# Kernel tuning notes

Hardware: AMD Instinct MI355X
Metric: run time of the kernel (lower is better)

The kernel has to match this reference:

```python
import jax, jax.numpy as jnp
import numpy as np

NUM_HIDDEN = 2048
NUM_CLASSES = 10
SEQ_LEN = 128
BATCH = 512


def setup_inputs() -> dict:
    key = jax.random.key(0)
    ks = jax.random.split(key, 6)
    # kaiming-uniform-ish init scales (exact init is irrelevant for correctness testing)
    def ku(k, shape, fan_in):
        bound = float(np.sqrt(6.0 / fan_in))
        return jax.random.uniform(k, shape, jnp.float32, -bound, bound)
    return {
        "x": jax.random.normal(ks[0], (BATCH, SEQ_LEN), jnp.float32),
        "weighthx": ku(ks[1], (NUM_HIDDEN, 1), 1),
        "weighthh": ku(ks[2], (NUM_HIDDEN, NUM_HIDDEN), NUM_HIDDEN),
        "bh": ku(ks[3], (NUM_HIDDEN, 1), 1),
        "weightph": ku(ks[4], (NUM_CLASSES, NUM_HIDDEN), NUM_HIDDEN),
        "bp": ku(ks[5], (NUM_CLASSES, 1), 1),
    }


def reference(x, weighthx, weighthh, bh, weightph, bp):
    # x: [B, S]; hidden state h: [H, B] as in the torch code
    B = x.shape[0]
    h0 = jnp.zeros((weighthh.shape[0], B), dtype=x.dtype)

    def step(h, xt):
        # xt: [B]; weighthx: [H, 1] -> input contribution [H, B]
        h_new = jnp.tanh(weighthx @ xt[None, :] + weighthh @ h + bh)
        return h_new, None

    h_final, _ = jax.lax.scan(step, h0, x.T)  # scan over S
    out = weightph @ h_final + bp  # [C, B]
    return out.T  # [B, C]
```

## Files before the change

### kernel.cpp

```cpp
#include <hip/hip_runtime.h>
#include <hip/hip_cooperative_groups.h>

#define HID 2048
#define BAT 512
#define SEQ 128
#define NCLS 10

typedef __attribute__((ext_vector_type(4))) float f32x4;
typedef __attribute__((ext_vector_type(8))) short s16x8;
typedef __attribute__((ext_vector_type(4))) unsigned short u16x4;

__device__ __forceinline__ float bf2f(unsigned short u) {
  union { unsigned int i; float f; } v;
  v.i = ((unsigned int)u) << 16;
  return v.f;
}
__device__ __forceinline__ unsigned short f2bf(float f) {
  union { float f; unsigned int i; } v;
  v.f = f;
  unsigned int u = v.i;
  return (unsigned short)((u + 0x7fffu + ((u >> 16) & 1u)) >> 16);
}

__global__ __launch_bounds__(256) void cvt_kernel(const float* __restrict__ src,
                                                  unsigned short* __restrict__ dst,
                                                  int n) {
  int i = (blockIdx.x * 256 + threadIdx.x) * 4;
  if (i + 3 < n) {
    f32x4 v = *(const f32x4*)(src + i);
    u16x4 o;
    o.x = f2bf(v.x);
    o.y = f2bf(v.y);
    o.z = f2bf(v.z);
    o.w = f2bf(v.w);
    *(u16x4*)(dst + i) = o;
  }
}

__global__ __launch_bounds__(256) void xpose_kernel(const float* __restrict__ x,
                                                    float* __restrict__ xT) {
  const int t = blockIdx.x;
  for (int b = threadIdx.x; b < BAT; b += 256)
    xT[t * BAT + b] = x[b * SEQ + t];
}

__device__ __forceinline__ void gload16(const void* g, void* l) {
  __builtin_amdgcn_global_load_lds(
      (const __attribute__((address_space(1))) unsigned int*)g,
      (__attribute__((address_space(3))) unsigned int*)l, 16, 0, 0);
}
__device__ __forceinline__ void gload16_dev(const void* g, void* l) {
  __builtin_amdgcn_global_load_lds(
      (const __attribute__((address_space(1))) unsigned int*)g,
      (__attribute__((address_space(3))) unsigned int*)l, 16, 0, 0x10);
}

__global__ __launch_bounds__(256) void rnn_kernel(
    const unsigned short* __restrict__ W,
    unsigned short* __restrict__ h0,
    unsigned short* __restrict__ h1,
    const float* __restrict__ whx,
    const float* __restrict__ bh,
    const float* __restrict__ xT,
    unsigned int* __restrict__ cnt) {
  __shared__ unsigned short ldsA[4][64 * 64];
  __shared__ unsigned short ldsB[4][64 * 64];

  const int tid = threadIdx.x;
  const int wave = tid >> 6;
  const int lane = tid & 63;
  const int id = blockIdx.x;
  const int g = id >> 5;
  const int m0 = (id & 31) * 64;
  const int n0 = g * 64;
  const int wm = wave >> 1;
  const int wn = wave & 1;
  const int fl = lane & 15;
  const int hi = lane >> 4;

  const int r0 = tid >> 3;
  const int r1 = 32 + r0;
  const int c0 = (tid & 7) ^ (r0 & 7);
  const int c1 = (tid & 7) ^ (r1 & 7);
  const unsigned short* gA0 = W + (size_t)(m0 + r0) * HID + c0 * 8;
  const unsigned short* gA1 = W + (size_t)(m0 + r1) * HID + c1 * 8;
  const size_t bo0 = (size_t)(n0 + r0) * HID + c0 * 8;
  const size_t bo1 = (size_t)(n0 + r1) * HID + c1 * 8;
  const int ldst = wave * 512;

  int offA[2][2], offB[2][2];
#pragma unroll
  for (int f = 0; f < 2; ++f) {
#pragma unroll
    for (int ks = 0; ks < 2; ++ks) {
      const int ra = wm * 32 + f * 16 + fl;
      const int rb = wn * 32 + f * 16 + fl;
      const int ch = ks * 4 + hi;
      offA[f][ks] = ra * 64 + ((ch ^ (ra & 7)) * 8);
      offB[f][ks] = rb * 64 + ((ch ^ (rb & 7)) * 8);
    }
  }

  const int mbase = m0 + wm * 32;
  const int nbase = n0 + wn * 32;
  f32x4 wxv[2], bvv[2];
#pragma unroll
  for (int mf = 0; mf < 2; ++mf) {
    wxv[mf] = *(const f32x4*)&whx[mbase + mf * 16 + hi * 4];
    bvv[mf] = *(const f32x4*)&bh[mbase + mf * 16 + hi * 4];
  }

  unsigned short* const A0 = ldsA[0]; unsigned short* const B0 = ldsB[0];
  unsigned short* const A1 = ldsA[1]; unsigned short* const B1 = ldsB[1];
  unsigned short* const A2 = ldsA[2]; unsigned short* const B2 = ldsB[2];
  unsigned short* const A3 = ldsA[3]; unsigned short* const B3 = ldsB[3];

#define STAGE(kk, ab, bb)                        \
  do {                                           \
    gload16(gA0 + (kk), (ab) + ldst);            \
    gload16(gA1 + (kk), (ab) + 2048 + ldst);     \
    gload16_dev(gB0 + (kk), (bb) + ldst);        \
    gload16_dev(gB1 + (kk), (bb) + 2048 + ldst); \
  } while (0)

#define COMPUTE(ab, bb)                                                                  \
  do {                                                                                   \
    _Pragma("unroll") for (int ks = 0; ks < 2; ++ks) {                                   \
      s16x8 a0 = *(const s16x8*)&(ab)[offA[0][ks]];                                      \
      s16x8 a1 = *(const s16x8*)&(ab)[offA[1][ks]];                                      \
      s16x8 b0 = *(const s16x8*)&(bb)[offB[0][ks]];                                      \
      s16x8 b1 = *(const s16x8*)&(bb)[offB[1][ks]];                                      \
      acc[0][0] = __builtin_amdgcn_mfma_f32_16x16x32_bf16(a0, b0, acc[0][0], 0, 0, 0);   \
      acc[0][1] = __builtin_amdgcn_mfma_f32_16x16x32_bf16(a0, b1, acc[0][1], 0, 0, 0);   \
      acc[1][0] = __builtin_amdgcn_mfma_f32_16x16x32_bf16(a1, b0, acc[1][0], 0, 0, 0);   \
      acc[1][1] = __builtin_amdgcn_mfma_f32_16x16x32_bf16(a1, b1, acc[1][1], 0, 0, 0);   \
    }                                                                                    \
  } while (0)

#define WAITB(n) \
  asm volatile("s_waitcnt vmcnt(" #n ") lgkmcnt(0)\n\ts_barrier" ::: "memory")

  for (int t = 0; t < SEQ; ++t) {
    const unsigned short* hin = (t & 1) ? h1 : h0;
    unsigned short* hout = (t & 1) ? h0 : h1;
    const unsigned short* gB0 = hin + bo0;
    const unsigned short* gB1 = hin + bo1;

    f32x4 acc[2][2] = {};

    STAGE(0, A0, B0);
    STAGE(64, A1, B1);
    STAGE(128, A2, B2);
    WAITB(8);

#pragma unroll 1
    for (int kb = 0; kb < 28; kb += 4) {
      const int k4 = kb * 64;
      STAGE(k4 + 192, A3, B3); COMPUTE(A0, B0); WAITB(8);
      STAGE(k4 + 256, A0, B0); COMPUTE(A1, B1); WAITB(8);
      STAGE(k4 + 320, A1, B1); COMPUTE(A2, B2); WAITB(8);
      STAGE(k4 + 384, A2, B2); COMPUTE(A3, B3); WAITB(8);
    }
    STAGE(1984, A3, B3);
    COMPUTE(A0, B0); WAITB(8);
    COMPUTE(A1, B1); WAITB(4);
    COMPUTE(A2, B2); WAITB(0);
    COMPUTE(A3, B3);

#pragma unroll
    for (int mf = 0; mf < 2; ++mf) {
      const int mrow = mbase + mf * 16 + hi * 4;
#pragma unroll
      for (int nf = 0; nf < 2; ++nf) {
        const int ncol = nbase + nf * 16 + fl;
        const float xv = xT[t * BAT + ncol];
        u16x4 o;
#pragma unroll
        for (int j = 0; j < 4; ++j) {
          float z = acc[mf][nf][j] + wxv[mf][j] * xv + bvv[mf][j];
          o[j] = f2bf(tanhf(z));
        }
        union { u16x4 v; unsigned long long u; } pun;
        pun.v = o;
        const unsigned long long addr =
            (unsigned long long)&hout[(size_t)ncol * HID + mrow];
        asm volatile("global_store_dwordx2 %0, %1, off sc1"
                     :: "v"(addr), "v"(pun.u) : "memory");
      }
    }

    if (t != SEQ - 1) {
      asm volatile("s_waitcnt vmcnt(0)" ::: "memory");
      __syncthreads();
      if (tid == 0) {
        __hip_atomic_fetch_add(&cnt[g * 16], 1u, __ATOMIC_RELAXED,
                               __HIP_MEMORY_SCOPE_AGENT);
        const unsigned int target = 32u * (unsigned)(t + 1);
        while (__hip_atomic_load(&cnt[g * 16], __ATOMIC_RELAXED,
                                 __HIP_MEMORY_SCOPE_AGENT) < target)
          __builtin_amdgcn_s_sleep(1);
      }
      __syncthreads();
    }
  }
#undef STAGE
#undef COMPUTE
#undef WAITB
}

__global__ __launch_bounds__(256) void proj_kernel(const unsigned short* __restrict__ hT,
                                                   const float* __restrict__ wp,
                                                   const float* __restrict__ bp,
                                                   float* __restrict__ out) {
  const int b = blockIdx.x;
  const int wave = threadIdx.x >> 6;
  const int lane = threadIdx.x & 63;
  for (int c = wave; c < NCLS; c += 4) {
    float s = 0.f;
    for (int k = lane * 8; k < HID; k += 512) {
      s16x8 hv = *(const s16x8*)&hT[b * HID + k];
      f32x4 w0 = *(const f32x4*)&wp[c * HID + k];
      f32x4 w1 = *(const f32x4*)&wp[c * HID + k + 4];
      s += w0.x * bf2f((unsigned short)hv[0]) + w0.y * bf2f((unsigned short)hv[1]) +
           w0.z * bf2f((unsigned short)hv[2]) + w0.w * bf2f((unsigned short)hv[3]) +
           w1.x * bf2f((unsigned short)hv[4]) + w1.y * bf2f((unsigned short)hv[5]) +
           w1.z * bf2f((unsigned short)hv[6]) + w1.w * bf2f((unsigned short)hv[7]);
    }
#pragma unroll
    for (int off = 32; off > 0; off >>= 1) s += __shfl_down(s, off);
    if (lane == 0) out[b * NCLS + c] = s + bp[c];
  }
}

extern "C" void kernel_launch(void* const* d_in, const int* in_sizes, int n_in,
                              void* d_out, int out_size, void* d_ws, size_t ws_size,
                              hipStream_t stream) {
  (void)in_sizes; (void)n_in; (void)out_size; (void)ws_size;
  const float* x   = (const float*)d_in[0];
  const float* whx = (const float*)d_in[1];
  const float* whh = (const float*)d_in[2];
  const float* bh  = (const float*)d_in[3];
  const float* wp  = (const float*)d_in[4];
  const float* bp  = (const float*)d_in[5];
  float* out = (float*)d_out;

  unsigned short* Wb = (unsigned short*)d_ws;
  unsigned short* h0 = Wb + (size_t)HID * HID;
  unsigned short* h1 = h0 + (size_t)BAT * HID;
  float* xT = (float*)(h1 + (size_t)BAT * HID);
  unsigned int* cnt = (unsigned int*)(xT + (size_t)SEQ * BAT);

  cvt_kernel<<<dim3((HID * HID) / 1024), 256, 0, stream>>>(whh, Wb, HID * HID);
  xpose_kernel<<<dim3(SEQ), 256, 0, stream>>>(x, xT);
  hipMemsetAsync(h0, 0, (size_t)BAT * HID * sizeof(unsigned short), stream);
  hipMemsetAsync(cnt, 0, 8 * 64, stream);

  const unsigned short* Wb_c = Wb;
  unsigned short* h0_p = h0;
  unsigned short* h1_p = h1;
  const float* whx_p = whx;
  const float* bh_p = bh;
  const float* xT_p = xT;
  unsigned int* cnt_p = cnt;
  void* args[] = {(void*)&Wb_c, (void*)&h0_p, (void*)&h1_p,
                  (void*)&whx_p, (void*)&bh_p, (void*)&xT_p, (void*)&cnt_p};
  hipLaunchCooperativeKernel((const void*)rnn_kernel, dim3(256), dim3(256),
                             args, 0, stream);

  proj_kernel<<<dim3(BAT), 256, 0, stream>>>(h0, wp, bp, out);
}
```

Baseline: 2.282 ms.

## Keep weight slab resident in LDS and stream hidden state from global into registers

Each block now loads its 32-row slice of the recurrent weight matrix into LDS once, before the time loop. The per-step work reads the hidden state from global memory directly into registers with software prefetch, so the weights are no longer re-streamed from global every step. The grid is repartitioned to 64 row-slices by 4 batch groups of 128 columns, and barrier targets change from 32 to 64 blocks per group. The sc1 inline-asm stores and per-step vmcnt waits are replaced with plain stores plus threadfences. The risks are that the hidden-state loads may not hit cache efficiently, the 128KB LDS allocation may limit occupancy or exceed limits, and the new fence semantics add ordering cost.

```diff
diff --git a/kernel.cpp b/kernel.cpp
--- a/kernel.cpp
+++ b/kernel.cpp
@@ -49,11 +49,6 @@
       (const __attribute__((address_space(1))) unsigned int*)g,
       (__attribute__((address_space(3))) unsigned int*)l, 16, 0, 0);
 }
-__device__ __forceinline__ void gload16_dev(const void* g, void* l) {
-  __builtin_amdgcn_global_load_lds(
-      (const __attribute__((address_space(1))) unsigned int*)g,
-      (__attribute__((address_space(3))) unsigned int*)l, 16, 0, 0x10);
-}
 
 __global__ __launch_bounds__(256) void rnn_kernel(
     const unsigned short* __restrict__ W,
@@ -63,116 +58,107 @@
     const float* __restrict__ bh,
     const float* __restrict__ xT,
     unsigned int* __restrict__ cnt) {
-  __shared__ unsigned short ldsA[4][64 * 64];
-  __shared__ unsigned short ldsB[4][64 * 64];
+  __shared__ unsigned short ldsW[32 * HID];
 
   const int tid = threadIdx.x;
   const int wave = tid >> 6;
   const int lane = tid & 63;
   const int id = blockIdx.x;
-  const int g = id >> 5;
-  const int m0 = (id & 31) * 64;
-  const int n0 = g * 64;
-  const int wm = wave >> 1;
-  const int wn = wave & 1;
+  const int mp = id >> 2;
+  const int g = id & 3;
+  const int n0 = g * 128;
   const int fl = lane & 15;
   const int hi = lane >> 4;
 
-  const int r0 = tid >> 3;
-  const int r1 = 32 + r0;
-  const int c0 = (tid & 7) ^ (r0 & 7);
-  const int c1 = (tid & 7) ^ (r1 & 7);
-  const unsigned short* gA0 = W + (size_t)(m0 + r0) * HID + c0 * 8;
-  const unsigned short* gA1 = W + (size_t)(m0 + r1) * HID + c1 * 8;
-  const size_t bo0 = (size_t)(n0 + r0) * HID + c0 * 8;
-  const size_t bo1 = (size_t)(n0 + r1) * HID + c1 * 8;
-  const int ldst = wave * 512;
-
-  int offA[2][2], offB[2][2];
-#pragma unroll
-  for (int f = 0; f < 2; ++f) {
+  {
+    const unsigned short* wp0 = W + (size_t)mp * 32 * HID;
+    for (int i = 0; i < 32; ++i) {
+      gload16(wp0 + (size_t)i * HID + ((tid ^ (i & 7)) * 8),
+              ldsW + i * HID + wave * 512);
+    }
+    asm volatile("s_waitcnt vmcnt(0)" ::: "memory");
+    __syncthreads();
+  }
+
+  int oA[2][2];
+#pragma unroll
+  for (int mf = 0; mf < 2; ++mf)
 #pragma unroll
     for (int ks = 0; ks < 2; ++ks) {
-      const int ra = wm * 32 + f * 16 + fl;
-      const int rb = wn * 32 + f * 16 + fl;
-      const int ch = ks * 4 + hi;
-      offA[f][ks] = ra * 64 + ((ch ^ (ra & 7)) * 8);
-      offB[f][ks] = rb * 64 + ((ch ^ (rb & 7)) * 8);
-    }
-  }
-
-  const int mbase = m0 + wm * 32;
-  const int nbase = n0 + wn * 32;
+      const int row = mf * 16 + fl;
+      oA[mf][ks] = row * HID + (((ks * 4 + hi) ^ (row & 7)) * 8);
+    }
+
+  size_t oB[2][2];
+#pragma unroll
+  for (int nf = 0; nf < 2; ++nf)
+#pragma unroll
+    for (int ks = 0; ks < 2; ++ks)
+      oB[nf][ks] =
+          (size_t)(n0 + wave * 32 + nf * 16 + fl) * HID + ks * 32 + hi * 8;
+
   f32x4 wxv[2], bvv[2];
 #pragma unroll
   for (int mf = 0; mf < 2; ++mf) {
-    wxv[mf] = *(const f32x4*)&whx[mbase + mf * 16 + hi * 4];
-    bvv[mf] = *(const f32x4*)&bh[mbase + mf * 16 + hi * 4];
-  }
-
-  unsigned short* const A0 = ldsA[0]; unsigned short* const B0 = ldsB[0];
-  unsigned short* const A1 = ldsA[1]; unsigned short* const B1 = ldsB[1];
-  unsigned short* const A2 = ldsA[2]; unsigned short* const B2 = ldsB[2];
-  unsigned short* const A3 = ldsA[3]; unsigned short* const B3 = ldsB[3];
-
-#define STAGE(kk, ab, bb)                        \
-  do {                                           \
-    gload16(gA0 + (kk), (ab) + ldst);            \
-    gload16(gA1 + (kk), (ab) + 2048 + ldst);     \
-    gload16_dev(gB0 + (kk), (bb) + ldst);        \
-    gload16_dev(gB1 + (kk), (bb) + 2048 + ldst); \
+    wxv[mf] = *(const f32x4*)&whx[mp * 32 + mf * 16 + hi * 4];
+    bvv[mf] = *(const f32x4*)&bh[mp * 32 + mf * 16 + hi * 4];
+  }
+
+#define LB(X, kk)                                        \
+  do {                                                   \
+    X##00 = *(const s16x8*)&hp[oB[0][0] + (kk) * 64];    \
+    X##01 = *(const s16x8*)&hp[oB[0][1] + (kk) * 64];    \
+    X##10 = *(const s16x8*)&hp[oB[1][0] + (kk) * 64];    \
+    X##11 = *(const s16x8*)&hp[oB[1][1] + (kk) * 64];    \
   } while (0)
 
-#define COMPUTE(ab, bb)                                                                  \
-  do {                                                                                   \
-    _Pragma("unroll") for (int ks = 0; ks < 2; ++ks) {                                   \
-      s16x8 a0 = *(const s16x8*)&(ab)[offA[0][ks]];                                      \
-      s16x8 a1 = *(const s16x8*)&(ab)[offA[1][ks]];                                      \
-      s16x8 b0 = *(const s16x8*)&(bb)[offB[0][ks]];                                      \
-      s16x8 b1 = *(const s16x8*)&(bb)[offB[1][ks]];                                      \
-      acc[0][0] = __builtin_amdgcn_mfma_f32_16x16x32_bf16(a0, b0, acc[0][0], 0, 0, 0);   \
-      acc[0][1] = __builtin_amdgcn_mfma_f32_16x16x32_bf16(a0, b1, acc[0][1], 0, 0, 0);   \
-      acc[1][0] = __builtin_amdgcn_mfma_f32_16x16x32_bf16(a1, b0, acc[1][0], 0, 0, 0);   \
-      acc[1][1] = __builtin_amdgcn_mfma_f32_16x16x32_bf16(a1, b1, acc[1][1], 0, 0, 0);   \
-    }                                                                                    \
+#define MF(X, kk)                                                                      \
+  do {                                                                                 \
+    const int ko = (kk) * 64;                                                          \
+    s16x8 a00 = *(const s16x8*)&ldsW[oA[0][0] + ko];                                   \
+    s16x8 a10 = *(const s16x8*)&ldsW[oA[1][0] + ko];                                   \
+    acc[0][0] = __builtin_amdgcn_mfma_f32_16x16x32_bf16(a00, X##00, acc[0][0], 0,0,0); \
+    acc[0][1] = __builtin_amdgcn_mfma_f32_16x16x32_bf16(a00, X##10, acc[0][1], 0,0,0); \
+    acc[1][0] = __builtin_amdgcn_mfma_f32_16x16x32_bf16(a10, X##00, acc[1][0], 0,0,0); \
+    acc[1][1] = __builtin_amdgcn_mfma_f32_16x16x32_bf16(a10, X##10, acc[1][1], 0,0,0); \
+    s16x8 a01 = *(const s16x8*)&ldsW[oA[0][1] + ko];                                   \
+    s16x8 a11 = *(const s16x8*)&ldsW[oA[1][1] + ko];                                   \
+    acc[0][0] = __builtin_amdgcn_mfma_f32_16x16x32_bf16(a01, X##01, acc[0][0], 0,0,0); \
+    acc[0][1] = __builtin_amdgcn_mfma_f32_16x16x32_bf16(a01, X##11, acc[0][1], 0,0,0); \
+    acc[1][0] = __builtin_amdgcn_mfma_f32_16x16x32_bf16(a11, X##01, acc[1][0], 0,0,0); \
+    acc[1][1] = __builtin_amdgcn_mfma_f32_16x16x32_bf16(a11, X##11, acc[1][1], 0,0,0); \
   } while (0)
 
-#define WAITB(n) \
-  asm volatile("s_waitcnt vmcnt(" #n ") lgkmcnt(0)\n\ts_barrier" ::: "memory")
-
   for (int t = 0; t < SEQ; ++t) {
-    const unsigned short* hin = (t & 1) ? h1 : h0;
-    unsigned short* hout = (t & 1) ? h0 : h1;
-    const unsigned short* gB0 = hin + bo0;
-    const unsigned short* gB1 = hin + bo1;
+    const unsigned short* hp = (t & 1) ? h1 : h0;
+    unsigned short* hq = (t & 1) ? h0 : h1;
 
     f32x4 acc[2][2] = {};
-
-    STAGE(0, A0, B0);
-    STAGE(64, A1, B1);
-    STAGE(128, A2, B2);
-    WAITB(8);
-
+    s16x8 BA00, BA01, BA10, BA11;
+    s16x8 BB00, BB01, BB10, BB11;
+    s16x8 BC00, BC01, BC10, BC11;
+    s16x8 BD00, BD01, BD10, BD11;
+
+    LB(BA, 0);
+    LB(BB, 1);
 #pragma unroll 1
     for (int kb = 0; kb < 28; kb += 4) {
-      const int k4 = kb * 64;
-      STAGE(k4 + 192, A3, B3); COMPUTE(A0, B0); WAITB(8);
-      STAGE(k4 + 256, A0, B0); COMPUTE(A1, B1); WAITB(8);
-      STAGE(k4 + 320, A1, B1); COMPUTE(A2, B2); WAITB(8);
-      STAGE(k4 + 384, A2, B2); COMPUTE(A3, B3); WAITB(8);
-    }
-    STAGE(1984, A3, B3);
-    COMPUTE(A0, B0); WAITB(8);
-    COMPUTE(A1, B1); WAITB(4);
-    COMPUTE(A2, B2); WAITB(0);
-    COMPUTE(A3, B3);
+      LB(BC, kb + 2); MF(BA, kb + 0);
+      LB(BD, kb + 3); MF(BB, kb + 1);
+      LB(BA, kb + 4); MF(BC, kb + 2);
+      LB(BB, kb + 5); MF(BD, kb + 3);
+    }
+    LB(BC, 30); MF(BA, 28);
+    LB(BD, 31); MF(BB, 29);
+    MF(BC, 30);
+    MF(BD, 31);
 
 #pragma unroll
     for (int mf = 0; mf < 2; ++mf) {
-      const int mrow = mbase + mf * 16 + hi * 4;
+      const int mrow = mp * 32 + mf * 16 + hi * 4;
 #pragma unroll
       for (int nf = 0; nf < 2; ++nf) {
-        const int ncol = nbase + nf * 16 + fl;
+        const int ncol = n0 + wave * 32 + nf * 16 + fl;
         const float xv = xT[t * BAT + ncol];
         u16x4 o;
 #pragma unroll
@@ -180,32 +166,27 @@
           float z = acc[mf][nf][j] + wxv[mf][j] * xv + bvv[mf][j];
           o[j] = f2bf(tanhf(z));
         }
-        union { u16x4 v; unsigned long long u; } pun;
-        pun.v = o;
-        const unsigned long long addr =
-            (unsigned long long)&hout[(size_t)ncol * HID + mrow];
-        asm volatile("global_store_dwordx2 %0, %1, off sc1"
-                     :: "v"(addr), "v"(pun.u) : "memory");
+        *(u16x4*)&hq[(size_t)ncol * HID + mrow] = o;
       }
     }
 
     if (t != SEQ - 1) {
-      asm volatile("s_waitcnt vmcnt(0)" ::: "memory");
+      __threadfence();
       __syncthreads();
       if (tid == 0) {
         __hip_atomic_fetch_add(&cnt[g * 16], 1u, __ATOMIC_RELAXED,
                                __HIP_MEMORY_SCOPE_AGENT);
-        const unsigned int target = 32u * (unsigned)(t + 1);
+        const unsigned int target = 64u * (unsigned)(t + 1);
         while (__hip_atomic_load(&cnt[g * 16], __ATOMIC_RELAXED,
                                  __HIP_MEMORY_SCOPE_AGENT) < target)
           __builtin_amdgcn_s_sleep(1);
       }
       __syncthreads();
-    }
-  }
-#undef STAGE
-#undef COMPUTE
-#undef WAITB
+      __threadfence();
+    }
+  }
+#undef LB
+#undef MF
 }
 
 __global__ __launch_bounds__(256) void proj_kernel(const unsigned short* __restrict__ hT,
```

After: 7.358 ms. 222% more time.
